# Kernel optimization log

Measured on AMD Instinct MI355X. Metric: run time of the kernel, lower is better.

The kernel has to match this reference:

```python
import jax, jax.numpy as jnp
import numpy as np

N = 100000   # nodes
E = 1600000  # edges
F = 128      # in = hidden channels
L = 4        # num GCN layers
G = 512      # graphs in batch
OUT = 10     # classes
EPS = 1e-5


def setup_inputs() -> dict:
    key = jax.random.key(0)
    ks = jax.random.split(key, 12)
    x = jax.random.normal(ks[0], (N, F), dtype=jnp.float32)
    edge_index = jax.random.randint(ks[1], (2, E), 0, N, dtype=jnp.int64)
    batch = jnp.sort(jax.random.randint(ks[2], (N,), 0, G, dtype=jnp.int64))
    s = 1.0 / np.sqrt(F)
    Ws = jax.random.uniform(ks[3], (L, F, F), jnp.float32, -s, s)
    bs = jax.random.uniform(ks[4], (L, F), jnp.float32, -s, s)
    gammas = jnp.ones((L, F), jnp.float32)
    betas = jnp.zeros((L, F), jnp.float32)
    s1 = 1.0 / np.sqrt(F * L)
    W1 = jax.random.uniform(ks[5], (F * L, F), jnp.float32, -s1, s1)
    b1 = jax.random.uniform(ks[6], (F,), jnp.float32, -s1, s1)
    g1 = jnp.ones((F,), jnp.float32)
    bt1 = jnp.zeros((F,), jnp.float32)
    s2 = 1.0 / np.sqrt(F)
    W2 = jax.random.uniform(ks[7], (F, OUT), jnp.float32, -s2, s2)
    b2 = jax.random.uniform(ks[8], (OUT,), jnp.float32, -s2, s2)
    return {"x": x, "edge_index": edge_index, "batch": batch, "Ws": Ws, "bs": bs,
            "gammas": gammas, "betas": betas, "W1": W1, "b1": b1, "g1": g1,
            "bt1": bt1, "W2": W2, "b2": b2}


def _batch_norm(x, g, b):
    # training-mode BatchNorm1d over the node dim (biased variance)
    mu = jnp.mean(x, axis=0)
    var = jnp.var(x, axis=0)
    return (x - mu) * jax.lax.rsqrt(var + EPS) * g + b


def reference(x, edge_index, batch, Ws, bs, gammas, betas, W1, b1, g1, bt1, W2, b2):
    row, col = edge_index[0], edge_index[1]
    # GCN normalization (add_self_loops=False since normalize=True)
    deg = jax.ops.segment_sum(jnp.ones((E,), x.dtype), col, num_segments=N)
    dinv = jnp.where(deg > 0, jax.lax.rsqrt(deg), 0.0)
    norm = dinv[row] * dinv[col]  # [E]
    pooled = []
    h = x
    for t in range(L):
        hw = h @ Ws[t]                                    # [N, F]
        msg = norm[:, None] * hw[row]                     # gather  [E, F]
        h = jax.ops.segment_sum(msg, col, num_segments=N) + bs[t]  # scatter [N, F]
        h = jax.nn.relu(h)
        h = _batch_norm(h, gammas[t], betas[t])
        pooled.append(jax.ops.segment_sum(h, batch, num_segments=G))  # [G, F]
    z = jnp.concatenate(pooled, axis=1)                   # [G, L*F]
    z = z @ W1 + b1
    z = _batch_norm(z, g1, bt1)
    z = jax.nn.relu(z)
    return z @ W2 + b2                                    # [G, OUT]
```

## Files before the change

### kernel.cpp

```cpp
#include <hip/hip_runtime.h>

#define NN 100000
#define EE 1600000
#define FF 128
#define LL 4
#define GG 512
#define OUTC 10
#define EPSF 1e-5f
#define NSCB ((NN + 255) / 256)

typedef __attribute__((ext_vector_type(8))) short short8;
typedef __attribute__((ext_vector_type(4))) float f32x4;

__device__ inline unsigned bf16rne(float f) {
  unsigned u = __float_as_uint(f);
  return (u + 0x7fffu + ((u >> 16) & 1u)) >> 16;
}
__device__ inline unsigned packbf(float lo, float hi) {
  return bf16rne(lo) | (bf16rne(hi) << 16);
}
__device__ inline float bflo(unsigned u) { return __uint_as_float(u << 16); }
__device__ inline float bfhi(unsigned u) { return __uint_as_float(u & 0xffff0000u); }


__global__ __launch_bounds__(256) void k_deg(const int* __restrict__ col, int* __restrict__ deg) {
  int e = blockIdx.x * 256 + threadIdx.x;
  if (e < EE) atomicAdd(&deg[col[e]], 1);
}

__global__ __launch_bounds__(256) void k_dinv(const int* __restrict__ deg, float* __restrict__ dinv) {
  int n = blockIdx.x * 256 + threadIdx.x;
  if (n < NN) {
    int d = deg[n];
    dinv[n] = d > 0 ? rsqrtf((float)d) : 0.0f;
  }
}

__global__ __launch_bounds__(256) void k_bsum(const int* __restrict__ deg, int* __restrict__ bsum) {
  int i = blockIdx.x * 256 + threadIdx.x;
  int v = (i < NN) ? deg[i] : 0;
#pragma unroll
  for (int off = 32; off > 0; off >>= 1) v += __shfl_down(v, off, 64);
  __shared__ int ws[4];
  if ((threadIdx.x & 63) == 0) ws[threadIdx.x >> 6] = v;
  __syncthreads();
  if (threadIdx.x == 0) bsum[blockIdx.x] = ws[0] + ws[1] + ws[2] + ws[3];
}

__global__ __launch_bounds__(256) void k_rowptr(const int* __restrict__ deg,
                                                const int* __restrict__ bsum,
                                                int* __restrict__ rowptr) {
  __shared__ int sb[512];
  __shared__ int sd[256];
  const int t = threadIdx.x;
  sb[t]       = (t < NSCB) ? bsum[t] : 0;
  sb[t + 256] = (t + 256 < NSCB) ? bsum[t + 256] : 0;
  __syncthreads();
#pragma unroll
  for (int off = 1; off < 512; off <<= 1) {
    int v0 = (t >= off) ? sb[t - off] : 0;
    int v1 = sb[t + 256 - off];
    __syncthreads();
    sb[t] += v0;
    sb[t + 256] += v1;
    __syncthreads();
  }
  const int bpre = (blockIdx.x == 0) ? 0 : sb[blockIdx.x - 1];
  const int i = blockIdx.x * 256 + t;
  const int d = (i < NN) ? deg[i] : 0;
  sd[t] = d;
  __syncthreads();
#pragma unroll
  for (int off = 1; off < 256; off <<= 1) {
    int v = (t >= off) ? sd[t - off] : 0;
    __syncthreads();
    sd[t] += v;
    __syncthreads();
  }
  if (i < NN) rowptr[i] = bpre + sd[t] - d;
  if (blockIdx.x == 0 && t == 0) rowptr[NN] = EE;
}

__global__ __launch_bounds__(256) void k_fill(const int* __restrict__ ei,
                                              const int* __restrict__ rowptr,
                                              int* __restrict__ cnt,
                                              const float* __restrict__ dinv,
                                              int2* __restrict__ ecw) {
  int e = blockIdx.x * 256 + threadIdx.x;
  if (e >= EE) return;
  int r = ei[e];
  int cl = ei[EE + e];
  int slot = rowptr[cl] + atomicAdd(&cnt[cl], 1);
  ecw[slot] = make_int2(r, __float_as_int(dinv[r] * dinv[cl]));
}

__global__ __launch_bounds__(256) void k_bounds(const int* __restrict__ batch, int* __restrict__ gstart) {
  int n = blockIdx.x * 256 + threadIdx.x;
  if (n >= NN) return;
  int b = batch[n];
  if (n == 0) {
    for (int g = 0; g <= b; ++g) gstart[g] = 0;
  } else {
    int bp = batch[n - 1];
    for (int g = bp + 1; g <= b; ++g) gstart[g] = n;
  }
  if (n == NN - 1) {
    for (int g = b + 1; g <= GG; ++g) gstart[g] = NN;
  }
}


__global__ __launch_bounds__(256) void k_cvt(const float* __restrict__ x, unsigned* __restrict__ Ab) {
  int i = blockIdx.x * 256 + threadIdx.x;
  if (i < NN * 64) {
    float2 v = *(const float2*)(x + (size_t)i * 2);
    Ab[i] = packbf(v.x, v.y);
  }
}

__global__ __launch_bounds__(256) void k_wcvt(const float* __restrict__ Ws, uint4* __restrict__ Wf) {
  int tid = blockIdx.x * 256 + threadIdx.x;
  int t = tid >> 12;
  int r = tid & 4095;
  int lane = r & 63;
  int which = (r >> 6) & 1;
  int ct = (r >> 7) & 7;
  int kc = r >> 10;
  int n = ct * 16 + (lane & 15);
  int k0 = kc * 32 + (lane >> 4) * 8;
  const float* W = Ws + t * 16384;
  unsigned h[8];
#pragma unroll
  for (int j = 0; j < 8; ++j) {
    float w = W[(k0 + j) * 128 + n];
    unsigned hb = bf16rne(w);
    if (which == 0) {
      h[j] = hb;
    } else {
      float hf = __uint_as_float(hb << 16);
      h[j] = bf16rne(w - hf);
    }
  }
  uint4 o;
  o.x = h[0] | (h[1] << 16);
  o.y = h[2] | (h[3] << 16);
  o.z = h[4] | (h[5] << 16);
  o.w = h[6] | (h[7] << 16);
  Wf[tid] = o;
}

__global__ __launch_bounds__(256) void k_mm(const unsigned* __restrict__ Ab,
                                            const uint4* __restrict__ Wf,
                                            unsigned* __restrict__ Bb) {
  const int lane = threadIdx.x & 63;
  const int w = threadIdx.x >> 6;
  const int quad = lane >> 4;
  const int m = lane & 15;
  const int rowbase = blockIdx.x * 64 + w * 16;
  const int arow = min(rowbase + m, NN - 1);
  const uint4* A4 = (const uint4*)Ab;
  f32x4 acc[8];
#pragma unroll
  for (int ct = 0; ct < 8; ++ct) acc[ct] = (f32x4){0.f, 0.f, 0.f, 0.f};
#pragma unroll
  for (int kc = 0; kc < 4; ++kc) {
    uint4 av = A4[arow * 16 + kc * 4 + quad];
    short8 af = *(short8*)&av;
#pragma unroll
    for (int ct = 0; ct < 8; ++ct) {
      uint4 bh = Wf[((kc * 8 + ct) * 2 + 0) * 64 + lane];
      uint4 bl = Wf[((kc * 8 + ct) * 2 + 1) * 64 + lane];
      acc[ct] = __builtin_amdgcn_mfma_f32_16x16x32_bf16(af, *(short8*)&bh, acc[ct], 0, 0, 0);
      acc[ct] = __builtin_amdgcn_mfma_f32_16x16x32_bf16(af, *(short8*)&bl, acc[ct], 0, 0, 0);
    }
  }
#pragma unroll
  for (int ct = 0; ct < 8; ++ct) {
#pragma unroll
    for (int r = 0; r < 4; ++r) {
      float v = acc[ct][r];
      float vo = __shfl_xor(v, 1);
      int row = rowbase + quad * 4 + r;
      if ((lane & 1) == 0 && row < NN) {
        Bb[row * 64 + ct * 8 + (m >> 1)] = packbf(v, vo);
      }
    }
  }
}

__global__ __launch_bounds__(256) void k_agg(const unsigned* __restrict__ Bb,
                                             const int* __restrict__ rowptr,
                                             const int2* __restrict__ ecw,
                                             const float* __restrict__ bias,
                                             float* __restrict__ Aout,
                                             float* __restrict__ bnbuf) {
  const int lane = threadIdx.x & 63;
  const int wave = threadIdx.x >> 6;
  const int c = lane * 2;
  const int gwave = blockIdx.x * 4 + wave;
  const int nwaves = gridDim.x * 4;
  const float2 bv = *(const float2*)(bias + c);
  float s0 = 0.f, s1 = 0.f, q0 = 0.f, q1 = 0.f;
  for (int n = gwave; n < NN; n += nwaves) {
    const int beg = rowptr[n];
    const int end = rowptr[n + 1];
    float ax[8], ay[8];
#pragma unroll
    for (int j = 0; j < 8; ++j) { ax[j] = 0.f; ay[j] = 0.f; }
    for (int base = beg; base < end; base += 32) {
      const int myj = base + lane;
      int msrc = 0;
      float mw = 0.f;
      if (lane < 32 && myj < end) {
        int2 p = ecw[myj];
        msrc = p.x;
        mw = __int_as_float(p.y);
      }
#pragma unroll
      for (int g = 0; g < 4; ++g) {
        if (base + g * 8 < end) {
          int is[8]; float wv[8]; unsigned us[8];
#pragma unroll
          for (int j = 0; j < 8; ++j) {
            is[j] = __shfl(msrc, g * 8 + j);
            wv[j] = __shfl(mw, g * 8 + j);
          }
#pragma unroll
          for (int j = 0; j < 8; ++j) us[j] = Bb[((unsigned)is[j] << 6) + (unsigned)lane];
#pragma unroll
          for (int j = 0; j < 8; ++j) {
            ax[j] = fmaf(wv[j], bflo(us[j]), ax[j]);
            ay[j] = fmaf(wv[j], bfhi(us[j]), ay[j]);
          }
        }
      }
    }
    float rx = ((ax[0] + ax[1]) + (ax[2] + ax[3])) + ((ax[4] + ax[5]) + (ax[6] + ax[7]));
    float ry = ((ay[0] + ay[1]) + (ay[2] + ay[3])) + ((ay[4] + ay[5]) + (ay[6] + ay[7]));
    rx = fmaxf(rx + bv.x, 0.f);
    ry = fmaxf(ry + bv.y, 0.f);
    *(float2*)(Aout + (size_t)n * FF + c) = make_float2(rx, ry);
    s0 += rx; s1 += ry;
    q0 = fmaf(rx, rx, q0); q1 = fmaf(ry, ry, q1);
  }
  __shared__ float sred[4][256];
  sred[wave][c] = s0;
  sred[wave][c + 1] = s1;
  sred[wave][128 + c] = q0;
  sred[wave][128 + c + 1] = q1;
  __syncthreads();
  const int t = threadIdx.x;
  float tot = sred[0][t] + sred[1][t] + sred[2][t] + sred[3][t];
  atomicAdd(&bnbuf[t], tot);
}

__global__ __launch_bounds__(128) void k_bnfin(const float* __restrict__ bnbuf,
                                               const float* __restrict__ gamma,
                                               const float* __restrict__ beta,
                                               float* __restrict__ bnsc) {
  const int c = threadIdx.x;
  float mu = bnbuf[c] * (1.0f / NN);
  float var = bnbuf[128 + c] * (1.0f / NN) - mu * mu;
  float inv = rsqrtf(var + EPSF);
  float sc = gamma[c] * inv;
  bnsc[c] = sc;
  bnsc[128 + c] = beta[c] - mu * sc;
}

__global__ __launch_bounds__(128) void k_bnapply(const float* __restrict__ A,
                                                 const float* __restrict__ bnsc,
                                                 const int* __restrict__ gstart,
                                                 float* __restrict__ pooledt,
                                                 unsigned* __restrict__ Ab) {
  const int g = blockIdx.x >> 3;
  const int sub = blockIdx.x & 7;
  const int s = gstart[g];
  const int e = gstart[g + 1];
  const int cnt = e - s;
  if (cnt <= 0) return;
  const int per = (cnt + 7) >> 3;
  const int ns = s + sub * per;
  const int ne = min(ns + per, e);
  if (ns >= ne) return;
  const int cp = threadIdx.x & 63;
  const int half = threadIdx.x >> 6;
  const float2 sc = *(const float2*)(bnsc + 2 * cp);
  const float2 sh = *(const float2*)(bnsc + 128 + 2 * cp);
  float accx = 0.f, accy = 0.f;
  for (int n = ns + half; n < ne; n += 2) {
    float2 v = *(const float2*)(A + (size_t)n * FF + 2 * cp);
    float vx = fmaf(v.x, sc.x, sh.x);
    float vy = fmaf(v.y, sc.y, sh.y);
    Ab[n * 64 + cp] = packbf(vx, vy);
    accx += vx;
    accy += vy;
  }
  atomicAdd(&pooledt[(size_t)g * 512 + 2 * cp], accx);
  atomicAdd(&pooledt[(size_t)g * 512 + 2 * cp + 1], accy);
}


__global__ __launch_bounds__(128) void k_z1(const float* __restrict__ pooled,
                                            const float* __restrict__ W1,
                                            const float* __restrict__ b1,
                                            float* __restrict__ z1) {
  __shared__ float sp[512];
  const int g = blockIdx.x;
  for (int i = threadIdx.x; i < 512; i += 128) sp[i] = pooled[(size_t)g * 512 + i];
  __syncthreads();
  const int c = threadIdx.x;
  float acc = b1[c];
  for (int j = 0; j < 512; ++j) acc = fmaf(sp[j], W1[j * 128 + c], acc);
  z1[(size_t)g * 128 + c] = acc;
}

__global__ __launch_bounds__(128) void k_zstat(const float* __restrict__ z1,
                                               const float* __restrict__ g1,
                                               const float* __restrict__ bt1,
                                               float* __restrict__ zsc) {
  const int c = threadIdx.x;
  float s = 0.f, q = 0.f;
  for (int g = 0; g < GG; ++g) {
    float v = z1[g * 128 + c];
    s += v;
    q = fmaf(v, v, q);
  }
  float mu = s * (1.0f / GG);
  float var = q * (1.0f / GG) - mu * mu;
  float inv = rsqrtf(var + EPSF);
  float sc = g1[c] * inv;
  zsc[c] = sc;
  zsc[128 + c] = bt1[c] - mu * sc;
}

__global__ __launch_bounds__(128) void k_out(const float* __restrict__ z1,
                                             const float* __restrict__ zsc,
                                             const float* __restrict__ W2,
                                             const float* __restrict__ b2,
                                             float* __restrict__ out) {
  __shared__ float zr[128];
  const int g = blockIdx.x;
  const int c = threadIdx.x;
  zr[c] = fmaxf(fmaf(z1[(size_t)g * 128 + c], zsc[c], zsc[128 + c]), 0.f);
  __syncthreads();
  if (c < OUTC) {
    float acc = b2[c];
    for (int k = 0; k < 128; ++k) acc = fmaf(zr[k], W2[k * OUTC + c], acc);
    out[(size_t)g * OUTC + c] = acc;
  }
}


extern "C" void kernel_launch(void* const* d_in, const int* in_sizes, int n_in,
                              void* d_out, int out_size, void* d_ws, size_t ws_size,
                              hipStream_t stream) {
  const float* x      = (const float*)d_in[0];
  const int*   ei     = (const int*)d_in[1];
  const int*   batch  = (const int*)d_in[2];
  const float* Ws     = (const float*)d_in[3];
  const float* bs     = (const float*)d_in[4];
  const float* gammas = (const float*)d_in[5];
  const float* betas  = (const float*)d_in[6];
  const float* W1     = (const float*)d_in[7];
  const float* b1     = (const float*)d_in[8];
  const float* g1     = (const float*)d_in[9];
  const float* bt1    = (const float*)d_in[10];
  const float* W2     = (const float*)d_in[11];
  const float* b2     = (const float*)d_in[12];
  float* out = (float*)d_out;

  char* ws = (char*)d_ws;
  size_t off = 0;
  auto alloc = [&](size_t bytes) -> void* {
    void* p = ws + off;
    off = (off + bytes + 255) & ~(size_t)255;
    return p;
  };
  int*   deg    = (int*)alloc((size_t)NN * 4);
  int*   cnt    = (int*)alloc((size_t)NN * 4);
  float* bnbuf  = (float*)alloc((size_t)LL * 256 * 4);
  float* pooled = (float*)alloc((size_t)GG * 512 * 4);
  size_t zero_bytes = off;
  float*    A      = (float*)alloc((size_t)NN * FF * 4);
  unsigned* Ab     = (unsigned*)alloc((size_t)NN * 64 * 4);
  unsigned* Bb     = (unsigned*)alloc((size_t)NN * 64 * 4);
  int2*     ecw    = (int2*)alloc((size_t)EE * 8);
  float*    dinv   = (float*)alloc((size_t)NN * 4);
  int*      rowptr = (int*)alloc((size_t)(NN + 1) * 4);
  int*      bsum   = (int*)alloc((size_t)NSCB * 4);
  int*      gstart = (int*)alloc((size_t)(GG + 1) * 4);
  uint4*    Wf     = (uint4*)alloc((size_t)LL * 4096 * 16);
  float*    z1     = (float*)alloc((size_t)GG * FF * 4);
  float*    bnsc   = (float*)alloc(256 * 4);
  float*    zsc    = (float*)alloc(256 * 4);
  (void)ws_size; (void)in_sizes; (void)n_in; (void)out_size;

  hipMemsetAsync(d_ws, 0, zero_bytes, stream);

  k_deg<<<(EE + 255) / 256, 256, 0, stream>>>(ei + EE, deg);
  k_dinv<<<(NN + 255) / 256, 256, 0, stream>>>(deg, dinv);
  k_bsum<<<NSCB, 256, 0, stream>>>(deg, bsum);
  k_rowptr<<<NSCB, 256, 0, stream>>>(deg, bsum, rowptr);
  k_fill<<<(EE + 255) / 256, 256, 0, stream>>>(ei, rowptr, cnt, dinv, ecw);
  k_bounds<<<(NN + 255) / 256, 256, 0, stream>>>(batch, gstart);
  k_cvt<<<(NN * 64 + 255) / 256, 256, 0, stream>>>(x, Ab);
  k_wcvt<<<64, 256, 0, stream>>>(Ws, Wf);

  for (int t = 0; t < LL; ++t) {
    k_mm<<<(NN + 63) / 64, 256, 0, stream>>>(Ab, Wf + (size_t)t * 4096, Bb);
    k_agg<<<2048, 256, 0, stream>>>(Bb, rowptr, ecw, bs + t * FF, A, bnbuf + t * 256);
    k_bnfin<<<1, 128, 0, stream>>>(bnbuf + t * 256, gammas + t * FF, betas + t * FF, bnsc);
    k_bnapply<<<GG * 8, 128, 0, stream>>>(A, bnsc, gstart, pooled + t * FF, Ab);
  }

  k_z1<<<GG, 128, 0, stream>>>(pooled, W1, b1, z1);
  k_zstat<<<1, 128, 0, stream>>>(z1, g1, bt1, zsc);
  k_out<<<GG, 128, 0, stream>>>(z1, zsc, W2, b2, out);
}
```

Measured before the change: 867.8 us.

## Store aggregation output as bf16 and widen edge batches with prefetch in k_agg

The aggregation kernel now writes its ReLU output as packed bf16 instead of fp32, which halves the intermediate buffer traffic between k_agg and k_bnapply. The edge loop also handles 64 edges per iteration using all lanes, prefetches the next chunk of edge records, and issues 16 gathers per group instead of 8 to raise memory-level parallelism. The cost is bf16 rounding of pre-norm activations, although BN statistics are still accumulated in fp32, and higher register pressure from the 16-wide unroll.

```diff
diff --git a/kernel.cpp b/kernel.cpp
--- a/kernel.cpp
+++ b/kernel.cpp
@@ -192,7 +192,7 @@
                                              const int* __restrict__ rowptr,
                                              const int2* __restrict__ ecw,
                                              const float* __restrict__ bias,
-                                             float* __restrict__ Aout,
+                                             unsigned* __restrict__ Ar,
                                              float* __restrict__ bnbuf) {
   const int lane = threadIdx.x & 63;
   const int wave = threadIdx.x >> 6;
@@ -207,30 +207,29 @@
     float ax[8], ay[8];
 #pragma unroll
     for (int j = 0; j < 8; ++j) { ax[j] = 0.f; ay[j] = 0.f; }
-    for (int base = beg; base < end; base += 32) {
-      const int myj = base + lane;
-      int msrc = 0;
-      float mw = 0.f;
-      if (lane < 32 && myj < end) {
-        int2 p = ecw[myj];
-        msrc = p.x;
-        mw = __int_as_float(p.y);
+    int2 stage = (beg + lane < end) ? ecw[beg + lane] : make_int2(0, 0);
+    for (int base = beg; base < end; base += 64) {
+      const int2 cur = stage;
+      const int nb = base + 64;
+      if (nb < end) {
+        const int j = nb + lane;
+        stage = (j < end) ? ecw[j] : make_int2(0, 0);
       }
 #pragma unroll
       for (int g = 0; g < 4; ++g) {
-        if (base + g * 8 < end) {
-          int is[8]; float wv[8]; unsigned us[8];
-#pragma unroll
-          for (int j = 0; j < 8; ++j) {
-            is[j] = __shfl(msrc, g * 8 + j);
-            wv[j] = __shfl(mw, g * 8 + j);
+        if (base + g * 16 < end) {
+          int is[16]; float wv[16]; unsigned us[16];
+#pragma unroll
+          for (int j = 0; j < 16; ++j) {
+            is[j] = __shfl(cur.x, g * 16 + j);
+            wv[j] = __shfl(__int_as_float(cur.y), g * 16 + j);
           }
 #pragma unroll
-          for (int j = 0; j < 8; ++j) us[j] = Bb[((unsigned)is[j] << 6) + (unsigned)lane];
-#pragma unroll
-          for (int j = 0; j < 8; ++j) {
-            ax[j] = fmaf(wv[j], bflo(us[j]), ax[j]);
-            ay[j] = fmaf(wv[j], bfhi(us[j]), ay[j]);
+          for (int j = 0; j < 16; ++j) us[j] = Bb[((unsigned)is[j] << 6) + (unsigned)lane];
+#pragma unroll
+          for (int j = 0; j < 16; ++j) {
+            ax[j & 7] = fmaf(wv[j], bflo(us[j]), ax[j & 7]);
+            ay[j & 7] = fmaf(wv[j], bfhi(us[j]), ay[j & 7]);
           }
         }
       }
@@ -239,7 +238,7 @@
     float ry = ((ay[0] + ay[1]) + (ay[2] + ay[3])) + ((ay[4] + ay[5]) + (ay[6] + ay[7]));
     rx = fmaxf(rx + bv.x, 0.f);
     ry = fmaxf(ry + bv.y, 0.f);
-    *(float2*)(Aout + (size_t)n * FF + c) = make_float2(rx, ry);
+    Ar[(size_t)n * 64 + lane] = packbf(rx, ry);
     s0 += rx; s1 += ry;
     q0 = fmaf(rx, rx, q0); q1 = fmaf(ry, ry, q1);
   }
@@ -267,7 +266,7 @@
   bnsc[128 + c] = beta[c] - mu * sc;
 }
 
-__global__ __launch_bounds__(128) void k_bnapply(const float* __restrict__ A,
+__global__ __launch_bounds__(128) void k_bnapply(const unsigned* __restrict__ Ar,
                                                  const float* __restrict__ bnsc,
                                                  const int* __restrict__ gstart,
                                                  float* __restrict__ pooledt,
@@ -288,10 +287,10 @@
   const float2 sh = *(const float2*)(bnsc + 128 + 2 * cp);
   float accx = 0.f, accy = 0.f;
   for (int n = ns + half; n < ne; n += 2) {
-    float2 v = *(const float2*)(A + (size_t)n * FF + 2 * cp);
-    float vx = fmaf(v.x, sc.x, sh.x);
-    float vy = fmaf(v.y, sc.y, sh.y);
-    Ab[n * 64 + cp] = packbf(vx, vy);
+    unsigned u = Ar[(size_t)n * 64 + cp];
+    float vx = fmaf(bflo(u), sc.x, sh.x);
+    float vy = fmaf(bfhi(u), sc.y, sh.y);
+    Ab[(size_t)n * 64 + cp] = packbf(vx, vy);
     accx += vx;
     accy += vy;
   }
@@ -381,7 +380,7 @@
   float* bnbuf  = (float*)alloc((size_t)LL * 256 * 4);
   float* pooled = (float*)alloc((size_t)GG * 512 * 4);
   size_t zero_bytes = off;
-  float*    A      = (float*)alloc((size_t)NN * FF * 4);
+  unsigned* Ar     = (unsigned*)alloc((size_t)NN * 64 * 4);
   unsigned* Ab     = (unsigned*)alloc((size_t)NN * 64 * 4);
   unsigned* Bb     = (unsigned*)alloc((size_t)NN * 64 * 4);
   int2*     ecw    = (int2*)alloc((size_t)EE * 8);
@@ -408,9 +407,9 @@
 
   for (int t = 0; t < LL; ++t) {
     k_mm<<<(NN + 63) / 64, 256, 0, stream>>>(Ab, Wf + (size_t)t * 4096, Bb);
-    k_agg<<<2048, 256, 0, stream>>>(Bb, rowptr, ecw, bs + t * FF, A, bnbuf + t * 256);
+    k_agg<<<2048, 256, 0, stream>>>(Bb, rowptr, ecw, bs + t * FF, Ar, bnbuf + t * 256);
     k_bnfin<<<1, 128, 0, stream>>>(bnbuf + t * 256, gammas + t * FF, betas + t * FF, bnsc);
-    k_bnapply<<<GG * 8, 128, 0, stream>>>(A, bnsc, gstart, pooled + t * FF, Ab);
+    k_bnapply<<<GG * 8, 128, 0, stream>>>(Ar, bnsc, gstart, pooled + t * FF, Ab);
   }
 
   k_z1<<<GG, 128, 0, stream>>>(pooled, W1, b1, z1);
```

Measured after the change: 858.2 us. About the same (-1.1%).
